# Kernel tuning notes

Measured on AMD Instinct MI355X. Metric: run time of the kernel, lower is better.

Reference implementation:

```python
import jax, jax.numpy as jnp
import numpy as np

H = 1024  # hidden size


def _gru_layer(x_seq, W_ih, W_hh, b_ih, b_hh):
    """Single GRU layer, PyTorch gate conventions.
    x_seq: (B, T, D_in). Returns full output sequence (B, T, H) and final h (B, H).
    """
    B = x_seq.shape[0]
    # Precompute input projections for all timesteps in one big GEMM: (B, T, 3H)
    xg = jnp.einsum('btd,gd->btg', x_seq, W_ih) + b_ih
    xg_t = jnp.swapaxes(xg, 0, 1)  # (T, B, 3H)

    def step(h, xg_step):
        hg = h @ W_hh.T + b_hh  # (B, 3H)
        xr, xz, xn = jnp.split(xg_step, 3, axis=-1)
        hr, hz, hn = jnp.split(hg, 3, axis=-1)
        r = jax.nn.sigmoid(xr + hr)
        z = jax.nn.sigmoid(xz + hz)
        n = jnp.tanh(xn + r * hn)
        h_new = (1.0 - z) * n + z * h
        return h_new, h_new

    h0 = jnp.zeros((B, H), dtype=x_seq.dtype)
    h_last, ys = jax.lax.scan(step, h0, xg_t)
    return jnp.swapaxes(ys, 0, 1), h_last  # (B, T, H), (B, H)


def setup_inputs() -> dict:
    key = jax.random.key(0)
    ks = jax.random.split(key, 8)
    s = 1.0 / np.sqrt(H)  # PyTorch-style init scale
    return {
        'x': jax.random.normal(ks[0], (64, 512, 118), dtype=jnp.float32),
        'W_ih0': jax.random.normal(ks[1], (3 * H, 118), dtype=jnp.float32) * s,
        'W_ih12': jax.random.normal(ks[2], (2, 3 * H, H), dtype=jnp.float32) * s,
        'W_hh': jax.random.normal(ks[3], (3, 3 * H, H), dtype=jnp.float32) * s,
        'b_ih': jax.random.normal(ks[4], (3, 3 * H), dtype=jnp.float32) * s,
        'b_hh': jax.random.normal(ks[5], (3, 3 * H), dtype=jnp.float32) * s,
        'W_lin': jax.random.normal(ks[6], (1, H), dtype=jnp.float32) * s,
        'b_lin': jax.random.normal(ks[7], (1,), dtype=jnp.float32) * s,
    }


def reference(x, W_ih0, W_ih12, W_hh, b_ih, b_hh, W_lin, b_lin):
    # Layer 0 (input dim 118)
    y, _ = _gru_layer(x, W_ih0, W_hh[0], b_ih[0], b_hh[0])
    # Layers 1, 2 (input dim H). Dropout disabled (eval-mode reference).
    y, _ = _gru_layer(y, W_ih12[0], W_hh[1], b_ih[1], b_hh[1])
    _, h_last = _gru_layer(y, W_ih12[1], W_hh[2], b_ih[2], b_hh[2])
    # Linear on last timestep of top layer: output[:, -1, :] == final hidden of layer 3
    return h_last @ W_lin.T + b_lin  # (B, 1)
```

## Files before the change

### kernel.cpp

```cpp
#include <hip/hip_runtime.h>

typedef _Float16 f16x8 __attribute__((ext_vector_type(8)));
typedef _Float16 f16x4 __attribute__((ext_vector_type(4)));
typedef float    f32x4 __attribute__((ext_vector_type(4)));

#define HID 1024
#define TT  512
#define BB  64
#define MROWS (TT*BB)
#define G3  (3*HID)
#define NWG 64
#define BH  (BB*HID)

__device__ __forceinline__ f32x4 mfma16(f16x8 a, f16x8 b, f32x4 c) {
  return __builtin_amdgcn_mfma_f32_16x16x32_f16(a, b, c, 0, 0, 0);
}

__device__ __forceinline__ void g2l16(const _Float16* g, _Float16* l) {
  __builtin_amdgcn_global_load_lds(
      (const __attribute__((address_space(1))) unsigned int*)g,
      (__attribute__((address_space(3))) unsigned int*)l, 16, 0, 0);
}

__device__ __forceinline__ float sigm(float x) { return 1.f / (1.f + __expf(-x)); }
__device__ __forceinline__ float tanh_f(float x) {
  x = fminf(fmaxf(x, -20.f), 20.f);
  float e = __expf(2.f * x);
  return (e - 1.f) / (e + 1.f);
}

#define H_LOAD16(dst, src) \
  asm volatile("global_load_dwordx4 %0, %1, off sc1" : "=v"(dst) : "v"(src))
#define H_STORE2(ptr, val16) \
  asm volatile("global_store_short %0, %1, off sc1" \
               :: "v"(ptr), "v"((unsigned)__builtin_bit_cast(unsigned short, (val16))) : "memory")
#define H_STORE16(ptr, v4) \
  asm volatile("global_store_dwordx4 %0, %1, off sc1" :: "v"(ptr), "v"(v4) : "memory")
#define WAIT_VM0 \
  do { asm volatile("s_waitcnt vmcnt(0)" ::: "memory"); } while (0)

__global__ __launch_bounds__(256) void prep_kernel(
    const float* __restrict__ x, const float* __restrict__ wih0,
    const float* __restrict__ wih12, const float* __restrict__ whh,
    _Float16* __restrict__ x16, _Float16* __restrict__ wi0_16,
    _Float16* __restrict__ wi12_16, _Float16* __restrict__ whh16,
    unsigned* __restrict__ flags)
{
  if (blockIdx.x == 0 && threadIdx.x < NWG) flags[threadIdx.x] = 0u;

  const int R0 = MROWS * 128;
  const int R1 = G3 * 128;
  const int R2 = 2 * G3 * HID;
  const int R3 = 3 * G3 * HID;
  const int total = R0 + R1 + R2 + R3;
  for (int idx = blockIdx.x * 256 + threadIdx.x; idx < total; idx += gridDim.x * 256) {
    if (idx < R0) {
      int row = idx >> 7, k = idx & 127;
      int t = row >> 6, b = row & 63;
      x16[idx] = (k < 118) ? (_Float16)x[((size_t)b * TT + t) * 118 + k] : (_Float16)0.f;
    } else if (idx < R0 + R1) {
      int i = idx - R0;
      int row = i >> 7, k = i & 127;
      wi0_16[i] = (k < 118) ? (_Float16)wih0[(size_t)row * 118 + k] : (_Float16)0.f;
    } else if (idx < R0 + R1 + R2) {
      int i = idx - (R0 + R1);
      wi12_16[i] = (_Float16)wih12[i];
    } else {
      int i = idx - (R0 + R1 + R2);
      whh16[i] = (_Float16)whh[i];
    }
  }
}

__global__ __launch_bounds__(256) void gemm_xg_kernel(
    const _Float16* __restrict__ A, const _Float16* __restrict__ W,
    const float* __restrict__ bias, _Float16* __restrict__ xg, int K)
{
  __shared__ __align__(16) _Float16 As[128 * 32];
  __shared__ __align__(16) _Float16 Bs[128 * 32];
  const int tid = threadIdx.x, l = tid & 63, wv = tid >> 6;
  const int wm = wv >> 1, wn = wv & 1;
  const size_t m0 = (size_t)blockIdx.y * 128, n0 = (size_t)blockIdx.x * 128;

  f32x4 acc[4][4];
#pragma unroll
  for (int i = 0; i < 4; ++i)
#pragma unroll
    for (int j = 0; j < 4; ++j) acc[i][j] = f32x4{0.f, 0.f, 0.f, 0.f};

  for (int kt = 0; kt < K; kt += 32) {
#pragma unroll
    for (int rr = 0; rr < 2; ++rr) {
      const int ca = rr * 256 + tid;
      const int row = ca >> 2, cir = ca & 3;
      const _Float16* ga = A + (m0 + row) * (size_t)K + kt + cir * 8;
      const _Float16* gb = W + (n0 + row) * (size_t)K + kt + cir * 8;
      _Float16* la = As + (rr * 256 + wv * 64) * 8;
      _Float16* lb = Bs + (rr * 256 + wv * 64) * 8;
      g2l16(ga, la);
      g2l16(gb, lb);
    }
    __syncthreads();
    f16x8 af[4], bf[4];
#pragma unroll
    for (int mt = 0; mt < 4; ++mt)
      af[mt] = *reinterpret_cast<const f16x8*>(As + (wm * 64 + mt * 16 + (l & 15)) * 32 + ((l >> 4) << 3));
#pragma unroll
    for (int nt = 0; nt < 4; ++nt)
      bf[nt] = *reinterpret_cast<const f16x8*>(Bs + (wn * 64 + nt * 16 + (l & 15)) * 32 + ((l >> 4) << 3));
#pragma unroll
    for (int mt = 0; mt < 4; ++mt)
#pragma unroll
      for (int nt = 0; nt < 4; ++nt)
        acc[mt][nt] = mfma16(af[mt], bf[nt], acc[mt][nt]);
    __syncthreads();
  }

  const int t0 = blockIdx.y * 2 + wm;
#pragma unroll
  for (int nt = 0; nt < 4; ++nt) {
    const int col = (int)n0 + wn * 64 + nt * 16 + (l & 15);
    const float bv = bias[col];
#pragma unroll
    for (int mt = 0; mt < 4; ++mt) {
      const int bq = mt * 16 + ((l >> 4) << 2);
      f16x4 o;
#pragma unroll
      for (int r = 0; r < 4; ++r) o[r] = (_Float16)(acc[mt][nt][r] + bv);
      *reinterpret_cast<f16x4*>(xg + ((size_t)t0 * G3 + col) * 64 + bq) = o;
    }
  }
}

#define MFMA_KB(kb, WCNT)                                                      \
  {                                                                            \
    asm volatile("s_waitcnt vmcnt(" WCNT ")" ::: "memory");                    \
    __builtin_amdgcn_sched_barrier(0);                                         \
    _Pragma("unroll")                                                          \
    for (int kk = 0; kk < 8; ++kk) {                                           \
      const int kbyte = ((kb) * 256 + kk * 32) * 2 + kqb;                      \
      _Pragma("unroll")                                                        \
      for (int gi = 0; gi < 3; ++gi) {                                         \
        const int lr = gi * 16 + (l & 15);                                     \
        const unsigned off = (unsigned)(lr * 2048 + kbyte) ^ (unsigned)((lr & 7) << 4); \
        f16x8 bfr = *reinterpret_cast<const f16x8*>(wl_b + off);               \
        acc[gi] = mfma16(afr[kb][kk], bfr, acc[gi]);                           \
      }                                                                        \
    }                                                                          \
  }

__global__ __launch_bounds__(256, 1) void gru_scan_kernel(
    const _Float16* __restrict__ xg,
    const _Float16* __restrict__ Wl,
    const float* __restrict__ bhh,
    _Float16* __restrict__ y16,
    float* h32L,
    _Float16* h16L,
    unsigned* flags,
    int steps, int t0g, int zero_h, unsigned g0)
{
  __shared__ __align__(16) _Float16 WL[48 * 1024];
  const int tid = threadIdx.x, l = tid & 63, w = tid >> 6;
  const int j0 = blockIdx.x * 16;
  char* wl_b = reinterpret_cast<char*>(WL);

  for (int c = tid; c < 48 * 128; c += 256) {
    const int lr = c >> 7, kc = c & 127;
    const int gi = lr >> 4, jr = lr & 15;
    const _Float16* src = Wl + (size_t)(gi * HID + j0 + jr) * HID + kc * 8;
    unsigned int byte = (unsigned)(lr * 2048 + kc * 16) ^ (unsigned)((lr & 7) << 4);
    *reinterpret_cast<uint4*>(wl_b + byte) = *reinterpret_cast<const uint4*>(src);
  }
  if (zero_h) {
    const int i = blockIdx.x * 256 + tid;
    f32x4 z = {0.f, 0.f, 0.f, 0.f};
    H_STORE16(reinterpret_cast<f32x4*>(h16L) + i, z);
  }

  const int jj = j0 + (l & 15);
  const int b0 = 16 * w + ((l >> 4) << 2);
  const float bhr = bhh[jj], bhz = bhh[HID + jj], bhn = bhh[2 * HID + jj];
  float hold[4];
#pragma unroll
  for (int r = 0; r < 4; ++r)
    hold[r] = zero_h ? 0.f : h32L[(size_t)(b0 + r) * HID + jj];
  const int arow = (16 * w + (l & 15)) * HID;
  const int kq = (l >> 4) << 3;
  const int kqb = kq * 2;

  unsigned gen = g0;
  WAIT_VM0;
  __syncthreads();
  if (tid == 0)
    __hip_atomic_store(&flags[blockIdx.x], gen, __ATOMIC_RELAXED, __HIP_MEMORY_SCOPE_AGENT);
  if (tid < NWG) {
    while (__hip_atomic_load(&flags[tid], __ATOMIC_RELAXED, __HIP_MEMORY_SCOPE_AGENT) < gen)
      __builtin_amdgcn_s_sleep(2);
  }
  __syncthreads();
  ++gen;

  f16x4 xr4, xz4, xn4;
  {
    const size_t xb = ((size_t)0 * G3 + jj) * 64 + b0;
    xr4 = *reinterpret_cast<const f16x4*>(xg + xb);
    xz4 = *reinterpret_cast<const f16x4*>(xg + xb + (size_t)HID * 64);
    xn4 = *reinterpret_cast<const f16x4*>(xg + xb + (size_t)2 * HID * 64);
  }

  for (int t = 0; t < steps; ++t) {
    const int p = (t0g + t) & 1;
    const _Float16* hr16 = h16L + (size_t)p * BH;
    _Float16* hw16 = h16L + (size_t)(p ^ 1) * BH;

    f32x4 acc[3];
#pragma unroll
    for (int gi = 0; gi < 3; ++gi) acc[gi] = f32x4{0.f, 0.f, 0.f, 0.f};

    f16x8 afr[4][8];
#pragma unroll
    for (int kb = 0; kb < 4; ++kb)
#pragma unroll
      for (int kk = 0; kk < 8; ++kk)
        H_LOAD16(afr[kb][kk], hr16 + arow + kq + kb * 256 + kk * 32);

    MFMA_KB(0, "24")
    MFMA_KB(1, "16")
    MFMA_KB(2, "8")
    MFMA_KB(3, "0")

    _Float16 hout[4];
#pragma unroll
    for (int r = 0; r < 4; ++r) {
      const float rg = sigm((float)xr4[r] + acc[0][r] + bhr);
      const float zg = sigm((float)xz4[r] + acc[1][r] + bhz);
      const float ng = tanh_f((float)xn4[r] + rg * (acc[2][r] + bhn));
      const float hv = (1.f - zg) * ng + zg * hold[r];
      hold[r] = hv;
      hout[r] = (_Float16)hv;
    }
#pragma unroll
    for (int r = 0; r < 4; ++r) H_STORE2(hw16 + (size_t)(b0 + r) * HID + jj, hout[r]);
    if (y16) {
#pragma unroll
      for (int r = 0; r < 4; ++r) y16[((size_t)t * BB + b0 + r) * HID + jj] = hout[r];
    }

    WAIT_VM0;
    __syncthreads();
    if (tid == 0)
      __hip_atomic_store(&flags[blockIdx.x], gen, __ATOMIC_RELAXED, __HIP_MEMORY_SCOPE_AGENT);
    if (t + 1 < steps) {
      const size_t xb = ((size_t)(t + 1) * G3 + jj) * 64 + b0;
      xr4 = *reinterpret_cast<const f16x4*>(xg + xb);
      xz4 = *reinterpret_cast<const f16x4*>(xg + xb + (size_t)HID * 64);
      xn4 = *reinterpret_cast<const f16x4*>(xg + xb + (size_t)2 * HID * 64);
    }
    if (tid < NWG) {
      while (__hip_atomic_load(&flags[tid], __ATOMIC_RELAXED, __HIP_MEMORY_SCOPE_AGENT) < gen)
        __builtin_amdgcn_s_sleep(2);
    }
    __syncthreads();
    ++gen;
  }

#pragma unroll
  for (int r = 0; r < 4; ++r) h32L[(size_t)(b0 + r) * HID + jj] = hold[r];
}

__global__ __launch_bounds__(256) void linear_kernel(
    const float* __restrict__ h32, const float* __restrict__ wlin,
    const float* __restrict__ blin, float* __restrict__ out)
{
  __shared__ float red[4];
  const int b = blockIdx.x, tid = threadIdx.x;
  float s = 0.f;
  for (int j = tid; j < HID; j += 256) s += h32[(size_t)b * HID + j] * wlin[j];
  for (int o = 32; o > 0; o >>= 1) s += __shfl_down(s, o);
  if ((tid & 63) == 0) red[tid >> 6] = s;
  __syncthreads();
  if (tid == 0) out[b] = red[0] + red[1] + red[2] + red[3] + blin[0];
}

extern "C" void kernel_launch(void* const* d_in, const int* in_sizes, int n_in,
                              void* d_out, int out_size, void* d_ws, size_t ws_size,
                              hipStream_t stream) {
  const float* x     = (const float*)d_in[0];
  const float* wih0  = (const float*)d_in[1];
  const float* wih12 = (const float*)d_in[2];
  const float* whh   = (const float*)d_in[3];
  const float* bih   = (const float*)d_in[4];
  const float* bhh   = (const float*)d_in[5];
  const float* wlin  = (const float*)d_in[6];
  const float* blin  = (const float*)d_in[7];
  float* out = (float*)d_out;

  const size_t fixedB = 8388608ull + 786432 + 12582912 + 18874368 + 786432 + 786432 + 1024;
  int C = 8;
  {
    const int cands[7] = {512, 256, 128, 64, 32, 16, 8};
    for (int i = 0; i < 7; ++i) {
      if (fixedB + (size_t)cands[i] * 524288ull <= ws_size) { C = cands[i]; break; }
    }
  }
  const int nch = TT / C;

  char* ws = (char*)d_ws;
  size_t o = 0;
  _Float16* XG  = (_Float16*)(ws + o); o += (size_t)C * G3 * BB * 2;
  _Float16* Ych = (_Float16*)(ws + o); o += (size_t)C * BB * HID * 2;
  _Float16* X16 = (_Float16*)(ws + o); o += (size_t)MROWS * 128 * 2;
  _Float16* WI0 = (_Float16*)(ws + o); o += (size_t)G3 * 128 * 2;
  _Float16* WI12= (_Float16*)(ws + o); o += (size_t)2 * G3 * HID * 2;
  _Float16* WHH = (_Float16*)(ws + o); o += (size_t)3 * G3 * HID * 2;
  _Float16* H16 = (_Float16*)(ws + o); o += (size_t)3 * 2 * BH * 2;
  float*    H32 = (float*)(ws + o);    o += (size_t)3 * BH * 4;
  unsigned* FLG = (unsigned*)(ws + o); o += 1024;

  prep_kernel<<<dim3(2048), dim3(256), 0, stream>>>(x, wih0, wih12, whh,
                                                    X16, WI0, WI12, WHH, FLG);

  unsigned g0 = 1;
  for (int c = 0; c < nch; ++c) {
    for (int layer = 0; layer < 3; ++layer) {
      const _Float16* A  = (layer == 0) ? X16 + (size_t)c * C * 64 * 128 : Ych;
      const int K        = (layer == 0) ? 128 : HID;
      const _Float16* WI = (layer == 0) ? WI0 : WI12 + (size_t)(layer - 1) * G3 * HID;
      gemm_xg_kernel<<<dim3(24, C / 2), dim3(256), 0, stream>>>(
          A, WI, bih + layer * G3, XG, K);

      gru_scan_kernel<<<dim3(NWG), dim3(256), 0, stream>>>(
          XG, WHH + (size_t)layer * G3 * HID, bhh + layer * G3,
          (layer < 2) ? Ych : (_Float16*)nullptr,
          H32 + (size_t)layer * BH, H16 + (size_t)layer * 2 * BH,
          FLG, C, c * C, (c == 0) ? 1 : 0, g0);
      g0 += (unsigned)(C + 1);
    }
  }

  linear_kernel<<<dim3(64), dim3(256), 0, stream>>>(H32 + 2 * (size_t)BH, wlin, blin, out);
}
```

Measured before the change: 11.63 ms.

## Fuse all three GRU layers into one wavefront-pipelined persistent scan kernel

Replaces the per-chunk sequence of input-projection GEMMs and per-layer scan launches with a single persistent kernel of 192 workgroups, 64 per layer. The layers run concurrently as a pipeline along time, synchronised by per-layer flag arrays and a ring buffer of layer outputs. Each step's input projection is computed inside the scan itself: layer 0 uses LDS-resident input weights, and layers 1 and 2 stream input weights from global memory each step. This removes many kernel launches and the staged xg round-trips, and overlaps the three recurrences. The cost is extra per-step global weight traffic for the upper layers, more flag-polling dependencies, and a deadlock risk if all 192 blocks are not co-resident.

```diff
diff --git a/kernel.cpp b/kernel.cpp
--- a/kernel.cpp
+++ b/kernel.cpp
@@ -1,7 +1,6 @@
 #include <hip/hip_runtime.h>
 
 typedef _Float16 f16x8 __attribute__((ext_vector_type(8)));
-typedef _Float16 f16x4 __attribute__((ext_vector_type(4)));
 typedef float    f32x4 __attribute__((ext_vector_type(4)));
 
 #define HID 1024
@@ -9,17 +8,10 @@
 #define BB  64
 #define MROWS (TT*BB)
 #define G3  (3*HID)
-#define NWG 64
 #define BH  (BB*HID)
 
 __device__ __forceinline__ f32x4 mfma16(f16x8 a, f16x8 b, f32x4 c) {
   return __builtin_amdgcn_mfma_f32_16x16x32_f16(a, b, c, 0, 0, 0);
-}
-
-__device__ __forceinline__ void g2l16(const _Float16* g, _Float16* l) {
-  __builtin_amdgcn_global_load_lds(
-      (const __attribute__((address_space(1))) unsigned int*)g,
-      (__attribute__((address_space(3))) unsigned int*)l, 16, 0, 0);
 }
 
 __device__ __forceinline__ float sigm(float x) { return 1.f / (1.f + __expf(-x)); }
@@ -34,8 +26,6 @@
 #define H_STORE2(ptr, val16) \
   asm volatile("global_store_short %0, %1, off sc1" \
                :: "v"(ptr), "v"((unsigned)__builtin_bit_cast(unsigned short, (val16))) : "memory")
-#define H_STORE16(ptr, v4) \
-  asm volatile("global_store_dwordx4 %0, %1, off sc1" :: "v"(ptr), "v"(v4) : "memory")
 #define WAIT_VM0 \
   do { asm volatile("s_waitcnt vmcnt(0)" ::: "memory"); } while (0)
 
@@ -46,7 +36,7 @@
     _Float16* __restrict__ wi12_16, _Float16* __restrict__ whh16,
     unsigned* __restrict__ flags)
 {
-  if (blockIdx.x == 0 && threadIdx.x < NWG) flags[threadIdx.x] = 0u;
+  if (blockIdx.x == 0 && threadIdx.x < 192) flags[threadIdx.x] = 0u;
 
   const int R0 = MROWS * 128;
   const int R1 = G3 * 128;
@@ -72,66 +62,6 @@
   }
 }
 
-__global__ __launch_bounds__(256) void gemm_xg_kernel(
-    const _Float16* __restrict__ A, const _Float16* __restrict__ W,
-    const float* __restrict__ bias, _Float16* __restrict__ xg, int K)
-{
-  __shared__ __align__(16) _Float16 As[128 * 32];
-  __shared__ __align__(16) _Float16 Bs[128 * 32];
-  const int tid = threadIdx.x, l = tid & 63, wv = tid >> 6;
-  const int wm = wv >> 1, wn = wv & 1;
-  const size_t m0 = (size_t)blockIdx.y * 128, n0 = (size_t)blockIdx.x * 128;
-
-  f32x4 acc[4][4];
-#pragma unroll
-  for (int i = 0; i < 4; ++i)
-#pragma unroll
-    for (int j = 0; j < 4; ++j) acc[i][j] = f32x4{0.f, 0.f, 0.f, 0.f};
-
-  for (int kt = 0; kt < K; kt += 32) {
-#pragma unroll
-    for (int rr = 0; rr < 2; ++rr) {
-      const int ca = rr * 256 + tid;
-      const int row = ca >> 2, cir = ca & 3;
-      const _Float16* ga = A + (m0 + row) * (size_t)K + kt + cir * 8;
-      const _Float16* gb = W + (n0 + row) * (size_t)K + kt + cir * 8;
-      _Float16* la = As + (rr * 256 + wv * 64) * 8;
-      _Float16* lb = Bs + (rr * 256 + wv * 64) * 8;
-      g2l16(ga, la);
-      g2l16(gb, lb);
-    }
-    __syncthreads();
-    f16x8 af[4], bf[4];
-#pragma unroll
-    for (int mt = 0; mt < 4; ++mt)
-      af[mt] = *reinterpret_cast<const f16x8*>(As + (wm * 64 + mt * 16 + (l & 15)) * 32 + ((l >> 4) << 3));
-#pragma unroll
-    for (int nt = 0; nt < 4; ++nt)
-      bf[nt] = *reinterpret_cast<const f16x8*>(Bs + (wn * 64 + nt * 16 + (l & 15)) * 32 + ((l >> 4) << 3));
-#pragma unroll
-    for (int mt = 0; mt < 4; ++mt)
-#pragma unroll
-      for (int nt = 0; nt < 4; ++nt)
-        acc[mt][nt] = mfma16(af[mt], bf[nt], acc[mt][nt]);
-    __syncthreads();
-  }
-
-  const int t0 = blockIdx.y * 2 + wm;
-#pragma unroll
-  for (int nt = 0; nt < 4; ++nt) {
-    const int col = (int)n0 + wn * 64 + nt * 16 + (l & 15);
-    const float bv = bias[col];
-#pragma unroll
-    for (int mt = 0; mt < 4; ++mt) {
-      const int bq = mt * 16 + ((l >> 4) << 2);
-      f16x4 o;
-#pragma unroll
-      for (int r = 0; r < 4; ++r) o[r] = (_Float16)(acc[mt][nt][r] + bv);
-      *reinterpret_cast<f16x4*>(xg + ((size_t)t0 * G3 + col) * 64 + bq) = o;
-    }
-  }
-}
-
 #define MFMA_KB(kb, WCNT)                                                      \
   {                                                                            \
     asm volatile("s_waitcnt vmcnt(" WCNT ")" ::: "memory");                    \
@@ -149,123 +79,194 @@
     }                                                                          \
   }
 
-__global__ __launch_bounds__(256, 1) void gru_scan_kernel(
-    const _Float16* __restrict__ xg,
-    const _Float16* __restrict__ Wl,
+__global__ __launch_bounds__(256, 1) void scan_all_kernel(
+    const _Float16* __restrict__ x16,
+    const _Float16* __restrict__ wi0,
+    const _Float16* __restrict__ wi12,
+    const _Float16* __restrict__ whh,
+    const float* __restrict__ bih,
     const float* __restrict__ bhh,
-    _Float16* __restrict__ y16,
-    float* h32L,
-    _Float16* h16L,
-    unsigned* flags,
-    int steps, int t0g, int zero_h, unsigned g0)
+    _Float16* y0,
+    _Float16* y1,
+    _Float16* h16_2,
+    float* h32,
+    unsigned* flt,
+    int rv)
 {
   __shared__ __align__(16) _Float16 WL[48 * 1024];
+  __shared__ __align__(16) _Float16 WI[48 * 128];
+  const int g  = blockIdx.x >> 6;
+  const int wg = blockIdx.x & 63;
+  const int j0 = wg * 16;
   const int tid = threadIdx.x, l = tid & 63, w = tid >> 6;
-  const int j0 = blockIdx.x * 16;
   char* wl_b = reinterpret_cast<char*>(WL);
-
-  for (int c = tid; c < 48 * 128; c += 256) {
-    const int lr = c >> 7, kc = c & 127;
-    const int gi = lr >> 4, jr = lr & 15;
-    const _Float16* src = Wl + (size_t)(gi * HID + j0 + jr) * HID + kc * 8;
-    unsigned int byte = (unsigned)(lr * 2048 + kc * 16) ^ (unsigned)((lr & 7) << 4);
-    *reinterpret_cast<uint4*>(wl_b + byte) = *reinterpret_cast<const uint4*>(src);
-  }
-  if (zero_h) {
-    const int i = blockIdx.x * 256 + tid;
-    f32x4 z = {0.f, 0.f, 0.f, 0.f};
-    H_STORE16(reinterpret_cast<f32x4*>(h16L) + i, z);
-  }
+  char* wi_b = reinterpret_cast<char*>(WI);
+  const int rmask = rv - 1;
+
+  {
+    const _Float16* Wl = whh + (size_t)g * G3 * HID;
+    for (int c = tid; c < 48 * 128; c += 256) {
+      const int lr = c >> 7, kc = c & 127;
+      const int gi = lr >> 4, jr = lr & 15;
+      const _Float16* src = Wl + (size_t)(gi * HID + j0 + jr) * HID + kc * 8;
+      unsigned byte = (unsigned)(lr * 2048 + kc * 16) ^ (unsigned)((lr & 7) << 4);
+      *reinterpret_cast<uint4*>(wl_b + byte) = *reinterpret_cast<const uint4*>(src);
+    }
+  }
+  if (g == 0) {
+    for (int c = tid; c < 48 * 16; c += 256) {
+      const int lr = c >> 4, kc = c & 15;
+      const int gi = lr >> 4, jr = lr & 15;
+      const _Float16* src = wi0 + (size_t)(gi * HID + j0 + jr) * 128 + kc * 8;
+      unsigned byte = (unsigned)(lr * 256 + kc * 16) ^ (unsigned)((lr & 7) << 4);
+      *reinterpret_cast<uint4*>(wi_b + byte) = *reinterpret_cast<const uint4*>(src);
+    }
+  }
+  __syncthreads();
+
+  unsigned* fltSelf = flt + g * 64;
+  unsigned* fltUp   = flt + (g - 1) * 64;
+  unsigned* fltDn   = flt + (g + 1) * 64;
+  _Float16* ySelf = (g == 0) ? y0 : y1;
+  const _Float16* yUp = (g == 1) ? y0 : y1;
+  const _Float16* wiL = wi12 + (size_t)(g - 1) * G3 * HID;
 
   const int jj = j0 + (l & 15);
   const int b0 = 16 * w + ((l >> 4) << 2);
-  const float bhr = bhh[jj], bhz = bhh[HID + jj], bhn = bhh[2 * HID + jj];
-  float hold[4];
-#pragma unroll
-  for (int r = 0; r < 4; ++r)
-    hold[r] = zero_h ? 0.f : h32L[(size_t)(b0 + r) * HID + jj];
+  const float bhr = bhh[g * G3 + jj], bhz = bhh[g * G3 + HID + jj], bhn = bhh[g * G3 + 2 * HID + jj];
+  const float bir = bih[g * G3 + jj], biz = bih[g * G3 + HID + jj], bin = bih[g * G3 + 2 * HID + jj];
   const int arow = (16 * w + (l & 15)) * HID;
   const int kq = (l >> 4) << 3;
   const int kqb = kq * 2;
-
-  unsigned gen = g0;
-  WAIT_VM0;
+  float hold[4] = {0.f, 0.f, 0.f, 0.f};
+
+  f32x4 acc_x[3];
+#define XG_PHASE(s)                                                                 \
+  {                                                                                 \
+    _Pragma("unroll")                                                               \
+    for (int gi = 0; gi < 3; ++gi) acc_x[gi] = f32x4{0.f, 0.f, 0.f, 0.f};           \
+    if (g == 0) {                                                                   \
+      f16x8 ax[4];                                                                  \
+      _Pragma("unroll")                                                             \
+      for (int kk = 0; kk < 4; ++kk)                                                \
+        ax[kk] = *reinterpret_cast<const f16x8*>(                                   \
+            x16 + ((size_t)(s)*BB + 16 * w + (l & 15)) * 128 + kk * 32 + kq);       \
+      _Pragma("unroll")                                                             \
+      for (int kk = 0; kk < 4; ++kk) {                                              \
+        _Pragma("unroll")                                                           \
+        for (int gi = 0; gi < 3; ++gi) {                                            \
+          const int lr = gi * 16 + (l & 15);                                        \
+          const unsigned off =                                                      \
+              (unsigned)(lr * 256 + (kk * 32 + kq) * 2) ^ (unsigned)((lr & 7) << 4);\
+          f16x8 bfr = *reinterpret_cast<const f16x8*>(wi_b + off);                  \
+          acc_x[gi] = mfma16(ax[kk], bfr, acc_x[gi]);                               \
+        }                                                                           \
+      }                                                                             \
+    } else {                                                                        \
+      const _Float16* ys = yUp + (size_t)((s)&rmask) * BH;                          \
+      f16x8 ay[4][8];                                                               \
+      _Pragma("unroll")                                                             \
+      for (int kb = 0; kb < 4; ++kb)                                                \
+        _Pragma("unroll")                                                           \
+        for (int kk = 0; kk < 8; ++kk)                                              \
+          H_LOAD16(ay[kb][kk], ys + arow + kq + kb * 256 + kk * 32);                \
+      WAIT_VM0;                                                                     \
+      __builtin_amdgcn_sched_barrier(0);                                            \
+      for (int kb = 0; kb < 4; ++kb) {                                              \
+        f16x8 bw[3][8];                                                             \
+        _Pragma("unroll")                                                           \
+        for (int gi = 0; gi < 3; ++gi)                                              \
+          _Pragma("unroll")                                                         \
+          for (int kk = 0; kk < 8; ++kk)                                            \
+            bw[gi][kk] = *reinterpret_cast<const f16x8*>(                           \
+                wiL + (size_t)(gi * HID + j0 + (l & 15)) * HID + kb * 256 + kk * 32 + kq); \
+        _Pragma("unroll")                                                           \
+        for (int kk = 0; kk < 8; ++kk)                                              \
+          _Pragma("unroll")                                                         \
+          for (int gi = 0; gi < 3; ++gi)                                            \
+            acc_x[gi] = mfma16(ay[kb][kk], bw[gi][kk], acc_x[gi]);                  \
+      }                                                                             \
+      WAIT_VM0;                                                                     \
+    }                                                                               \
+  }
+
+  if (g > 0 && tid < 64) {
+    while (__hip_atomic_load(&fltUp[tid], __ATOMIC_RELAXED, __HIP_MEMORY_SCOPE_AGENT) < 1u)
+      __builtin_amdgcn_s_sleep(1);
+  }
   __syncthreads();
-  if (tid == 0)
-    __hip_atomic_store(&flags[blockIdx.x], gen, __ATOMIC_RELAXED, __HIP_MEMORY_SCOPE_AGENT);
-  if (tid < NWG) {
-    while (__hip_atomic_load(&flags[tid], __ATOMIC_RELAXED, __HIP_MEMORY_SCOPE_AGENT) < gen)
-      __builtin_amdgcn_s_sleep(2);
-  }
-  __syncthreads();
-  ++gen;
-
-  f16x4 xr4, xz4, xn4;
-  {
-    const size_t xb = ((size_t)0 * G3 + jj) * 64 + b0;
-    xr4 = *reinterpret_cast<const f16x4*>(xg + xb);
-    xz4 = *reinterpret_cast<const f16x4*>(xg + xb + (size_t)HID * 64);
-    xn4 = *reinterpret_cast<const f16x4*>(xg + xb + (size_t)2 * HID * 64);
-  }
-
-  for (int t = 0; t < steps; ++t) {
-    const int p = (t0g + t) & 1;
-    const _Float16* hr16 = h16L + (size_t)p * BH;
-    _Float16* hw16 = h16L + (size_t)(p ^ 1) * BH;
+  XG_PHASE(0)
+
+  for (int t = 0; t < TT; ++t) {
+    if (tid < 64) {
+      if (t >= 1) {
+        while (__hip_atomic_load(&fltSelf[tid], __ATOMIC_RELAXED, __HIP_MEMORY_SCOPE_AGENT) < (unsigned)t)
+          __builtin_amdgcn_s_sleep(1);
+      }
+      if (g < 2 && t >= rv) {
+        while (__hip_atomic_load(&fltDn[tid], __ATOMIC_RELAXED, __HIP_MEMORY_SCOPE_AGENT) < (unsigned)(t - rv + 1))
+          __builtin_amdgcn_s_sleep(1);
+      }
+    }
+    __syncthreads();
 
     f32x4 acc[3];
 #pragma unroll
     for (int gi = 0; gi < 3; ++gi) acc[gi] = f32x4{0.f, 0.f, 0.f, 0.f};
 
-    f16x8 afr[4][8];
-#pragma unroll
-    for (int kb = 0; kb < 4; ++kb)
-#pragma unroll
-      for (int kk = 0; kk < 8; ++kk)
-        H_LOAD16(afr[kb][kk], hr16 + arow + kq + kb * 256 + kk * 32);
-
-    MFMA_KB(0, "24")
-    MFMA_KB(1, "16")
-    MFMA_KB(2, "8")
-    MFMA_KB(3, "0")
+    if (t >= 1) {
+      const _Float16* hsrc = (g == 2) ? h16_2 + (size_t)(t & 1) * BH
+                                      : ySelf + (size_t)((t - 1) & rmask) * BH;
+      f16x8 afr[4][8];
+#pragma unroll
+      for (int kb = 0; kb < 4; ++kb)
+#pragma unroll
+        for (int kk = 0; kk < 8; ++kk)
+          H_LOAD16(afr[kb][kk], hsrc + arow + kq + kb * 256 + kk * 32);
+      MFMA_KB(0, "24")
+      MFMA_KB(1, "16")
+      MFMA_KB(2, "8")
+      MFMA_KB(3, "0")
+    }
 
     _Float16 hout[4];
 #pragma unroll
     for (int r = 0; r < 4; ++r) {
-      const float rg = sigm((float)xr4[r] + acc[0][r] + bhr);
-      const float zg = sigm((float)xz4[r] + acc[1][r] + bhz);
-      const float ng = tanh_f((float)xn4[r] + rg * (acc[2][r] + bhn));
+      const float rg = sigm(acc_x[0][r] + bir + acc[0][r] + bhr);
+      const float zg = sigm(acc_x[1][r] + biz + acc[1][r] + bhz);
+      const float ng = tanh_f(acc_x[2][r] + bin + rg * (acc[2][r] + bhn));
       const float hv = (1.f - zg) * ng + zg * hold[r];
       hold[r] = hv;
       hout[r] = (_Float16)hv;
     }
-#pragma unroll
-    for (int r = 0; r < 4; ++r) H_STORE2(hw16 + (size_t)(b0 + r) * HID + jj, hout[r]);
-    if (y16) {
-#pragma unroll
-      for (int r = 0; r < 4; ++r) y16[((size_t)t * BB + b0 + r) * HID + jj] = hout[r];
+    if (g == 2) {
+#pragma unroll
+      for (int r = 0; r < 4; ++r)
+        H_STORE2(h16_2 + (size_t)((t & 1) ^ 1) * BH + (size_t)(b0 + r) * HID + jj, hout[r]);
+      if (t == TT - 1) {
+#pragma unroll
+        for (int r = 0; r < 4; ++r) h32[(size_t)(b0 + r) * HID + jj] = hold[r];
+      }
+    } else {
+#pragma unroll
+      for (int r = 0; r < 4; ++r)
+        H_STORE2(ySelf + (size_t)(t & rmask) * BH + (size_t)(b0 + r) * HID + jj, hout[r]);
     }
 
     WAIT_VM0;
     __syncthreads();
     if (tid == 0)
-      __hip_atomic_store(&flags[blockIdx.x], gen, __ATOMIC_RELAXED, __HIP_MEMORY_SCOPE_AGENT);
-    if (t + 1 < steps) {
-      const size_t xb = ((size_t)(t + 1) * G3 + jj) * 64 + b0;
-      xr4 = *reinterpret_cast<const f16x4*>(xg + xb);
-      xz4 = *reinterpret_cast<const f16x4*>(xg + xb + (size_t)HID * 64);
-      xn4 = *reinterpret_cast<const f16x4*>(xg + xb + (size_t)2 * HID * 64);
-    }
-    if (tid < NWG) {
-      while (__hip_atomic_load(&flags[tid], __ATOMIC_RELAXED, __HIP_MEMORY_SCOPE_AGENT) < gen)
-        __builtin_amdgcn_s_sleep(2);
-    }
-    __syncthreads();
-    ++gen;
-  }
-
-#pragma unroll
-  for (int r = 0; r < 4; ++r) h32L[(size_t)(b0 + r) * HID + jj] = hold[r];
+      __hip_atomic_store(&fltSelf[wg], (unsigned)(t + 1), __ATOMIC_RELAXED, __HIP_MEMORY_SCOPE_AGENT);
+
+    if (t + 1 < TT) {
+      if (g > 0 && tid < 64) {
+        while (__hip_atomic_load(&fltUp[tid], __ATOMIC_RELAXED, __HIP_MEMORY_SCOPE_AGENT) < (unsigned)(t + 2))
+          __builtin_amdgcn_s_sleep(1);
+      }
+      __syncthreads();
+      XG_PHASE(t + 1)
+    }
+  }
 }
 
 __global__ __launch_bounds__(256) void linear_kernel(
@@ -295,48 +296,32 @@
   const float* blin  = (const float*)d_in[7];
   float* out = (float*)d_out;
 
-  const size_t fixedB = 8388608ull + 786432 + 12582912 + 18874368 + 786432 + 786432 + 1024;
-  int C = 8;
+  const size_t fixedB = 8388608ull + 786432 + 12582912 + 18874368 + 262144 + 262144 + 1024;
+  int rv = 32;
   {
-    const int cands[7] = {512, 256, 128, 64, 32, 16, 8};
-    for (int i = 0; i < 7; ++i) {
-      if (fixedB + (size_t)cands[i] * 524288ull <= ws_size) { C = cands[i]; break; }
-    }
-  }
-  const int nch = TT / C;
+    const int cands[4] = {256, 128, 64, 32};
+    for (int i = 0; i < 4; ++i) {
+      if (fixedB + 2ull * (size_t)cands[i] * 131072ull <= ws_size) { rv = cands[i]; break; }
+    }
+  }
 
   char* ws = (char*)d_ws;
   size_t o = 0;
-  _Float16* XG  = (_Float16*)(ws + o); o += (size_t)C * G3 * BB * 2;
-  _Float16* Ych = (_Float16*)(ws + o); o += (size_t)C * BB * HID * 2;
   _Float16* X16 = (_Float16*)(ws + o); o += (size_t)MROWS * 128 * 2;
   _Float16* WI0 = (_Float16*)(ws + o); o += (size_t)G3 * 128 * 2;
   _Float16* WI12= (_Float16*)(ws + o); o += (size_t)2 * G3 * HID * 2;
   _Float16* WHH = (_Float16*)(ws + o); o += (size_t)3 * G3 * HID * 2;
-  _Float16* H16 = (_Float16*)(ws + o); o += (size_t)3 * 2 * BH * 2;
-  float*    H32 = (float*)(ws + o);    o += (size_t)3 * BH * 4;
-  unsigned* FLG = (unsigned*)(ws + o); o += 1024;
+  _Float16* H162= (_Float16*)(ws + o); o += (size_t)2 * BH * 2;
+  float*    H32 = (float*)(ws + o);    o += (size_t)BH * 4;
+  unsigned* FLT = (unsigned*)(ws + o); o += 1024;
+  _Float16* Y0  = (_Float16*)(ws + o); o += (size_t)rv * BH * 2;
+  _Float16* Y1  = (_Float16*)(ws + o); o += (size_t)rv * BH * 2;
 
   prep_kernel<<<dim3(2048), dim3(256), 0, stream>>>(x, wih0, wih12, whh,
-                                                    X16, WI0, WI12, WHH, FLG);
-
-  unsigned g0 = 1;
-  for (int c = 0; c < nch; ++c) {
-    for (int layer = 0; layer < 3; ++layer) {
-      const _Float16* A  = (layer == 0) ? X16 + (size_t)c * C * 64 * 128 : Ych;
-      const int K        = (layer == 0) ? 128 : HID;
-      const _Float16* WI = (layer == 0) ? WI0 : WI12 + (size_t)(layer - 1) * G3 * HID;
-      gemm_xg_kernel<<<dim3(24, C / 2), dim3(256), 0, stream>>>(
-          A, WI, bih + layer * G3, XG, K);
-
-      gru_scan_kernel<<<dim3(NWG), dim3(256), 0, stream>>>(
-          XG, WHH + (size_t)layer * G3 * HID, bhh + layer * G3,
-          (layer < 2) ? Ych : (_Float16*)nullptr,
-          H32 + (size_t)layer * BH, H16 + (size_t)layer * 2 * BH,
-          FLG, C, c * C, (c == 0) ? 1 : 0, g0);
-      g0 += (unsigned)(C + 1);
-    }
-  }
-
-  linear_kernel<<<dim3(64), dim3(256), 0, stream>>>(H32 + 2 * (size_t)BH, wlin, blin, out);
-}
+                                                    X16, WI0, WI12, WHH, FLT);
+
+  scan_all_kernel<<<dim3(192), dim3(256), 0, stream>>>(
+      X16, WI0, WI12, WHH, bih, bhh, Y0, Y1, H162, H32, FLT, rv);
+
+  linear_kernel<<<dim3(64), dim3(256), 0, stream>>>(H32, wlin, blin, out);
+}
```

Result: faster. 10.95 ms (-5.9%).
